# Kernel optimization log

Hardware: AMD Instinct MI355X
Metric: run time of the kernel (lower is better)

Reference implementation:

```python
import jax, jax.numpy as jnp
import numpy as np

NVAR, B, C, H, W = 3, 4, 256, 64, 64
C1 = C // 2          # dat channels (nc)
C2 = C - C1
HEADS = 4
HC = C1 // HEADS     # head channels
STRIDE = 4
KS = 4
HK, WK = H // STRIDE, W // STRIDE
NS = HK * WK         # n_sample
RPE_H, RPE_W = 2 * H - 1, 2 * W - 1
NPAIR = 3


def _grid_sample(img, grid):
    # img [B,C,Hi,Wi]; grid [B,Hg,Wg,2] = (x,y) in [-1,1]; bilinear, align_corners=True, zero-pad
    Bn, Cn, Hi, Wi = img.shape
    x = (grid[..., 0] + 1.0) * 0.5 * (Wi - 1)
    y = (grid[..., 1] + 1.0) * 0.5 * (Hi - 1)
    x0 = jnp.floor(x)
    y0 = jnp.floor(y)
    wx = x - x0
    wy = y - y0
    x0i = x0.astype(jnp.int32)
    y0i = y0.astype(jnp.int32)
    imt = img.transpose(0, 2, 3, 1)  # [B,Hi,Wi,C]
    bidx = jnp.arange(Bn)[:, None, None]

    def corner(yi, xi, wgt):
        ok = ((xi >= 0) & (xi < Wi) & (yi >= 0) & (yi < Hi)).astype(img.dtype)
        val = imt[bidx, jnp.clip(yi, 0, Hi - 1), jnp.clip(xi, 0, Wi - 1)]  # [B,Hg,Wg,C]
        return val * (wgt * ok)[..., None]

    out = (corner(y0i, x0i, (1 - wx) * (1 - wy))
           + corner(y0i, x0i + 1, wx * (1 - wy))
           + corner(y0i + 1, x0i, (1 - wx) * wy)
           + corner(y0i + 1, x0i + 1, wx * wy))
    return out.transpose(0, 3, 1, 2)  # [B,C,Hg,Wg]


def _ref_points(hk, wk):
    # normalized sampling-grid reference points, (y,x) order
    ry = (jnp.linspace(0.5, hk - 0.5, hk) / (hk - 1.0)) * 2.0 - 1.0
    rx = (jnp.linspace(0.5, wk - 0.5, wk) / (wk - 1.0)) * 2.0 - 1.0
    return jnp.stack(jnp.meshgrid(ry, rx, indexing='ij'), axis=-1)  # [hk,wk,2]


def _q_grid(h, w):
    gy = (jnp.arange(h, dtype=jnp.float32) / (h - 1.0)) * 2.0 - 1.0
    gx = (jnp.arange(w, dtype=jnp.float32) / (w - 1.0)) * 2.0 - 1.0
    return jnp.stack(jnp.meshgrid(gy, gx, indexing='ij'), axis=-1).reshape(h * w, 2)


def _conv1x1(x, w, b=None):
    y = jnp.einsum('oc,bchw->bohw', w, x)
    return y if b is None else y + b[None, :, None, None]


def _dat_block(q_in, kv_in, pWq, pbq, pWk, pbk, pWv, pbv, pWo, pbo,
               pdw_w, pdw_b, pln_g, pln_b, ppw_w, prpe):
    Bn = q_in.shape[0]
    q = _conv1x1(q_in, pWq, pbq)  # [B,C1,H,W]
    # offset net: depthwise 4x4 stride-4 conv -> channel LN -> GELU -> 1x1 conv to 2
    off = jax.lax.conv_general_dilated(
        q, pdw_w, (STRIDE, STRIDE), 'VALID',
        dimension_numbers=('NCHW', 'OIHW', 'NCHW'),
        feature_group_count=C1) + pdw_b[None, :, None, None]  # [B,C1,HK,WK]
    mu = off.mean(axis=1, keepdims=True)
    var = ((off - mu) ** 2).mean(axis=1, keepdims=True)
    off = (off - mu) * jax.lax.rsqrt(var + 1e-5) * pln_g[None, :, None, None] + pln_b[None, :, None, None]
    off = jax.nn.gelu(off, approximate=False)
    offset = _conv1x1(off, ppw_w).transpose(0, 2, 3, 1)  # [B,HK,WK,2] (dy,dx)
    # offset_range_factor = -1 -> no tanh scaling, clamp pos into [-1,1]
    pos = jnp.clip(offset + _ref_points(HK, WK)[None], -1.0, 1.0)  # [B,HK,WK,2]
    xs = _grid_sample(kv_in, pos[..., ::-1])  # sample kv at deformed points -> [B,C1,HK,WK]
    k = _conv1x1(xs, pWk, pbk).reshape(Bn, HEADS, HC, NS)
    v = _conv1x1(xs, pWv, pbv).reshape(Bn, HEADS, HC, NS)
    qh = q.reshape(Bn, HEADS, HC, H * W)
    attn = jnp.einsum('bhcm,bhcn->bhmn', qh, k) * (HC ** -0.5)  # [B,h,HW,NS]
    # relative position bias sampled from rpe table
    disp = (_q_grid(H, W)[None, :, None, :] - pos.reshape(Bn, 1, NS, 2)) * 0.5  # [B,HW,NS,2]
    rpe_b = jnp.broadcast_to(prpe[None], (Bn, HEADS, RPE_H, RPE_W))
    bias = _grid_sample(rpe_b, disp[..., ::-1])  # [B,h,HW,NS]
    attn = jax.nn.softmax(attn + bias, axis=-1)
    out = jnp.einsum('bhmn,bhcn->bhcm', attn, v).reshape(Bn, C1, H, W)
    return _conv1x1(out, pWo, pbo)


def _forward(xs, params):
    results = []
    num = 0
    for i in range(NVAR):
        res = xs[i]
        for j in range(i):
            attn_out = _dat_block(xs[i][:, :C1], xs[j][:, :C1],
                                  *(p[num] for p in params))
            # torch: res -= -cat(zeros[:,:C2], attn)  => add attn on channels C2:
            res = res.at[:, C2:].add(attn_out)
            num += 1
        results.append(res)
    return jnp.stack(results)  # [NVAR,B,C,H,W]


def setup_inputs() -> dict:
    key = jax.random.key(0)
    ks = jax.random.split(key, 4)
    d = {}
    for n, k in zip(['x0', 'x1', 'x2'], jax.random.split(ks[0], 3)):
        d[n] = jax.random.normal(k, (B, C, H, W), jnp.float32)

    def w(k, shape, s=0.02):
        return jax.random.normal(k, shape, jnp.float32) * s

    kk = jax.random.split(ks[1], 8)
    d['Wq'] = w(kk[0], (NPAIR, C1, C1))
    d['bq'] = jnp.zeros((NPAIR, C1), jnp.float32)
    d['Wk'] = w(kk[1], (NPAIR, C1, C1))
    d['bk'] = jnp.zeros((NPAIR, C1), jnp.float32)
    d['Wv'] = w(kk[2], (NPAIR, C1, C1))
    d['bv'] = jnp.zeros((NPAIR, C1), jnp.float32)
    d['Wo'] = w(kk[3], (NPAIR, C1, C1))
    d['bo'] = jnp.zeros((NPAIR, C1), jnp.float32)
    d['dw_w'] = w(kk[4], (NPAIR, C1, 1, KS, KS), 0.1)
    d['dw_b'] = jnp.zeros((NPAIR, C1), jnp.float32)
    d['ln_g'] = jnp.ones((NPAIR, C1), jnp.float32)
    d['ln_b'] = jnp.zeros((NPAIR, C1), jnp.float32)
    d['pw_w'] = w(kk[5], (NPAIR, 2, C1), 0.1)
    d['rpe'] = w(kk[6], (NPAIR, HEADS, RPE_H, RPE_W), 0.01)
    return d


def reference(x0, x1, x2, Wq, bq, Wk, bk, Wv, bv, Wo, bo,
              dw_w, dw_b, ln_g, ln_b, pw_w, rpe):
    params = (Wq, bq, Wk, bk, Wv, bv, Wo, bo, dw_w, dw_b, ln_g, ln_b, pw_w, rpe)
    out = _forward([x0, x1, x2], params)
    flow = jnp.zeros((NVAR, x0.shape[0]), out.dtype)
    return out, flow
```

## Files before the change

kernel.cpp:

```cpp
#include <hip/hip_runtime.h>
#include <math.h>

#define NVAR 3
#define BB 4
#define CC 256
#define C1 128
#define HEADS 4
#define HH 64
#define WW 64
#define HW 4096
#define RPE_W 127
#define NP 3
#define SCALE 0.17677669529663687f

typedef short bf16x8 __attribute__((ext_vector_type(8)));
typedef float f32x4 __attribute__((ext_vector_type(4)));
typedef __bf16 bf16x2 __attribute__((ext_vector_type(2)));

__device__ __forceinline__ unsigned short f2bf(float f) {
    unsigned int u = __float_as_uint(f);
    u += 0x7fffu + ((u >> 16) & 1u);
    return (unsigned short)(u >> 16);
}
__device__ __forceinline__ float bflo(unsigned u) { return __uint_as_float(u << 16); }
__device__ __forceinline__ float bfhi(unsigned u) { return __uint_as_float(u & 0xffff0000u); }

__device__ __forceinline__ float dot2bf(unsigned a, unsigned b, float c) {
#if __has_builtin(__builtin_amdgcn_fdot2_f32_bf16)
    return __builtin_amdgcn_fdot2_f32_bf16(__builtin_bit_cast(bf16x2, a),
                                           __builtin_bit_cast(bf16x2, b), c, false);
#else
    return c + bflo(a) * bflo(b) + bfhi(a) * bfhi(b);
#endif
}

__global__ __launch_bounds__(256) void prep_copy(const float* __restrict__ rpe,
                                                 const float* __restrict__ Wq,
                                                 const float* __restrict__ Wo,
                                                 const float* __restrict__ Wk,
                                                 const float* __restrict__ Wv,
                                                 const float* __restrict__ x0,
                                                 unsigned short* __restrict__ tabbf,
                                                 unsigned short* __restrict__ wqh,
                                                 unsigned short* __restrict__ wql,
                                                 unsigned short* __restrict__ woh,
                                                 unsigned short* __restrict__ wkh,
                                                 unsigned short* __restrict__ wvh,
                                                 float* __restrict__ out) {
    int blk = blockIdx.x;
    if (blk >= 24) {
        const long long n4 = (long long)BB * CC * HW / 4;
        long long i = (long long)(blk - 24) * 256 + threadIdx.x;
        const long long stride = 1024LL * 256;
        for (; i < n4 + 12; i += stride) {
            if (i < n4) ((float4*)out)[i] = ((const float4*)x0)[i];
            else out[3LL * BB * CC * HW + (i - n4)] = 0.f;
        }
        return;
    }
    if (blk < 12) {
        const float* src = rpe + (long long)blk * RPE_W * RPE_W;
        unsigned short* dst = tabbf + (long long)blk * 16384;
        for (int idx = threadIdx.x; idx < 16384; idx += 256) {
            int y = idx >> 7, x = idx & 127;
            float v = (y < RPE_W && x < RPE_W) ? src[y * RPE_W + x] : 0.f;
            dst[idx] = f2bf(v);
        }
    } else if (blk < 15) {
        int p = blk - 12;
        for (int i = threadIdx.x; i < 16384; i += 256) {
            float w = Wq[p * 16384 + i];
            unsigned short h = f2bf(w);
            wqh[p * 16384 + i] = h;
            wql[p * 16384 + i] = f2bf(w - bflo((unsigned)h));
        }
    } else if (blk < 18) {
        int p = blk - 15;
        for (int i = threadIdx.x; i < 16384; i += 256)
            woh[p * 16384 + i] = f2bf(Wo[p * 16384 + i]);
    } else if (blk < 21) {
        int p = blk - 18;
        for (int i = threadIdx.x; i < 16384; i += 256)
            wkh[p * 16384 + i] = f2bf(Wk[p * 16384 + i]);
    } else {
        int p = blk - 21;
        for (int i = threadIdx.x; i < 16384; i += 256)
            wvh[p * 16384 + i] = f2bf(Wv[p * 16384 + i]);
    }
}

__global__ __launch_bounds__(256) void conv_q(const float* __restrict__ x1,
                                              const float* __restrict__ x2,
                                              const unsigned short* __restrict__ wqh,
                                              const unsigned short* __restrict__ wql,
                                              const float* __restrict__ bq,
                                              float* __restrict__ qbuf,
                                              unsigned short* __restrict__ qbf,
                                              float* __restrict__ out) {
    __shared__ unsigned short qlds[4][16][136];
    int wid = threadIdx.x >> 6, lane = threadIdx.x & 63;
    int g = lane >> 4, lm = lane & 15;
    int gw = blockIdx.x * 4 + wid;
    int mt = gw & 255;
    int pb = gw >> 8;
    int p = pb >> 2, b = pb & 3;
    const float* X = ((p == 0) ? x1 : x2) + (long long)b * CC * HW;
    int m = mt * 16 + lm;
    float* outc = (p < 2)
        ? out + (((long long)((p + 1) * 4 + b)) * CC) * HW + m
        : nullptr;

    bf16x8 bhi[4], blo[4];
#pragma unroll
    for (int ksl = 0; ksl < 4; ksl++) {
        float v[8];
#pragma unroll
        for (int j = 0; j < 8; j++) {
            int k = ksl * 32 + 8 * g + j;
            v[j] = X[(long long)k * HW + m];
            if (outc) outc[(long long)k * HW] = v[j];
        }
        union { unsigned u[4]; bf16x8 v; } H, L;
#pragma unroll
        for (int t = 0; t < 4; t++) {
            unsigned short h0 = f2bf(v[2 * t]), h1 = f2bf(v[2 * t + 1]);
            unsigned short l0 = f2bf(v[2 * t] - bflo((unsigned)h0));
            unsigned short l1 = f2bf(v[2 * t + 1] - bflo((unsigned)h1));
            H.u[t] = (unsigned)h0 | ((unsigned)h1 << 16);
            L.u[t] = (unsigned)l0 | ((unsigned)l1 << 16);
        }
        bhi[ksl] = H.v;
        blo[ksl] = L.v;
    }

    const unsigned short* WH = wqh + p * 16384;
    const unsigned short* WL = wql + p * 16384;
    unsigned short* ql = &qlds[wid][lm][0];
    f32x4 zero = {0.f, 0.f, 0.f, 0.f};
#pragma unroll
    for (int ct2 = 0; ct2 < 4; ct2++) {
        int ct0 = 2 * ct2, ct1 = ct0 + 1;
        f32x4 a0 = zero, a1 = zero;
#pragma unroll
        for (int ksl = 0; ksl < 4; ksl++) {
            bf16x8 Ah0 = *(const bf16x8*)(WH + (ct0 * 16 + lm) * 128 + ksl * 32 + 8 * g);
            bf16x8 Al0 = *(const bf16x8*)(WL + (ct0 * 16 + lm) * 128 + ksl * 32 + 8 * g);
            bf16x8 Ah1 = *(const bf16x8*)(WH + (ct1 * 16 + lm) * 128 + ksl * 32 + 8 * g);
            bf16x8 Al1 = *(const bf16x8*)(WL + (ct1 * 16 + lm) * 128 + ksl * 32 + 8 * g);
            a0 = __builtin_amdgcn_mfma_f32_16x16x32_bf16(Ah0, bhi[ksl], a0, 0, 0, 0);
            a1 = __builtin_amdgcn_mfma_f32_16x16x32_bf16(Ah1, bhi[ksl], a1, 0, 0, 0);
            a0 = __builtin_amdgcn_mfma_f32_16x16x32_bf16(Ah0, blo[ksl], a0, 0, 0, 0);
            a1 = __builtin_amdgcn_mfma_f32_16x16x32_bf16(Ah1, blo[ksl], a1, 0, 0, 0);
            a0 = __builtin_amdgcn_mfma_f32_16x16x32_bf16(Al0, bhi[ksl], a0, 0, 0, 0);
            a1 = __builtin_amdgcn_mfma_f32_16x16x32_bf16(Al1, bhi[ksl], a1, 0, 0, 0);
        }
        float q0[4], q1[4];
#pragma unroll
        for (int r = 0; r < 4; r++) {
            int c0 = ct0 * 16 + 4 * g + r, c1 = ct1 * 16 + 4 * g + r;
            q0[r] = a0[r] + bq[p * 128 + c0];
            q1[r] = a1[r] + bq[p * 128 + c1];
            qbuf[((long long)pb * 128 + c0) * HW + m] = q0[r];
            qbuf[((long long)pb * 128 + c1) * HW + m] = q1[r];
        }
        *(unsigned*)(ql + ct0 * 16 + 4 * g) =
            (unsigned)f2bf(q0[0] * SCALE) | ((unsigned)f2bf(q0[1] * SCALE) << 16);
        *(unsigned*)(ql + ct0 * 16 + 4 * g + 2) =
            (unsigned)f2bf(q0[2] * SCALE) | ((unsigned)f2bf(q0[3] * SCALE) << 16);
        *(unsigned*)(ql + ct1 * 16 + 4 * g) =
            (unsigned)f2bf(q1[0] * SCALE) | ((unsigned)f2bf(q1[1] * SCALE) << 16);
        *(unsigned*)(ql + ct1 * 16 + 4 * g + 2) =
            (unsigned)f2bf(q1[2] * SCALE) | ((unsigned)f2bf(q1[3] * SCALE) << 16);
    }

    unsigned short* Yb = qbf + ((long long)pb * HW + mt * 16) * 128;
    int q = lane >> 4, cg = lane & 15;
#pragma unroll
    for (int i = 0; i < 4; i++) {
        int row = i * 4 + q;
        uint4 vv = *(const uint4*)&qlds[wid][row][cg * 8];
        *(uint4*)(Yb + row * 128 + cg * 8) = vv;
    }
}

__global__ __launch_bounds__(256) void mid_kernel(const float* __restrict__ qbuf,
                                                  const float* __restrict__ dw_w,
                                                  const float* __restrict__ dw_b,
                                                  const float* __restrict__ ln_g,
                                                  const float* __restrict__ ln_b,
                                                  const float* __restrict__ pw_w,
                                                  const float* __restrict__ x0,
                                                  const float* __restrict__ x1,
                                                  float* __restrict__ posb,
                                                  uint4* __restrict__ prmb,
                                                  unsigned short* __restrict__ xT) {
    __shared__ float sm[32 * 4 * 65 + 16 * 128];
    int blk = blockIdx.x;
    int tid = threadIdx.x;
    if (blk < 192) {
        float (*ld)[4][65] = (float(*)[4][65])sm;
        float (*dwout)[128] = (float(*)[128])(sm + 32 * 4 * 65);
        int pb = blk >> 4, hk = blk & 15;
        int p = pb >> 2;
        for (int cq = 0; cq < 4; cq++) {
            int c32 = cq * 32;
            __syncthreads();
#pragma unroll
            for (int it = 0; it < 8; it++) {
                int i2 = tid + it * 256;
                int c = i2 >> 6, rem = i2 & 63;
                int y = rem >> 4, xq = rem & 15;
                float4 v = *(const float4*)(qbuf + ((long long)pb * 128 + c32 + c) * HW
                                            + (4 * hk + y) * 64 + xq * 4);
                ld[c][y][xq * 4 + 0] = v.x;
                ld[c][y][xq * 4 + 1] = v.y;
                ld[c][y][xq * 4 + 2] = v.z;
                ld[c][y][xq * 4 + 3] = v.w;
            }
            __syncthreads();
            int wk = tid >> 4;
#pragma unroll
            for (int oi = 0; oi < 2; oi++) {
                int c = (tid & 15) + oi * 16;
                const float* dwp = dw_w + (p * 128 + c32 + c) * 16;
                float acc = dw_b[p * 128 + c32 + c];
#pragma unroll
                for (int ky = 0; ky < 4; ky++)
#pragma unroll
                    for (int kx = 0; kx < 4; kx++)
                        acc += ld[c][ky][wk * 4 + kx] * dwp[ky * 4 + kx];
                dwout[wk][c32 + c] = acc;
            }
        }
        __syncthreads();
        int wid = tid >> 6, lane = tid & 63;
        for (int i = 0; i < 4; i++) {
            int wk = wid * 4 + i;
            int s = hk * 16 + wk;
            float a0 = dwout[wk][lane], a1 = dwout[wk][lane + 64];
            float s1 = a0 + a1;
#pragma unroll
            for (int o = 1; o < 64; o <<= 1) s1 += __shfl_xor(s1, o);
            float mu = s1 * (1.f / 128.f);
            float d0 = a0 - mu, d1 = a1 - mu;
            float v2 = d0 * d0 + d1 * d1;
#pragma unroll
            for (int o = 1; o < 64; o <<= 1) v2 += __shfl_xor(v2, o);
            float rs = rsqrtf(v2 * (1.f / 128.f) + 1e-5f);
            int c0 = lane, c1 = lane + 64;
            float y0 = d0 * rs * ln_g[p * 128 + c0] + ln_b[p * 128 + c0];
            float y1 = d1 * rs * ln_g[p * 128 + c1] + ln_b[p * 128 + c1];
            float g0 = 0.5f * y0 * (1.f + erff(y0 * 0.70710678118654752f));
            float g1 = 0.5f * y1 * (1.f + erff(y1 * 0.70710678118654752f));
            float o0 = pw_w[(p * 2 + 0) * 128 + c0] * g0
                     + pw_w[(p * 2 + 0) * 128 + c1] * g1;
            float o1 = pw_w[(p * 2 + 1) * 128 + c0] * g0
                     + pw_w[(p * 2 + 1) * 128 + c1] * g1;
#pragma unroll
            for (int o = 1; o < 64; o <<= 1) o0 += __shfl_xor(o0, o);
#pragma unroll
            for (int o = 1; o < 64; o <<= 1) o1 += __shfl_xor(o1, o);
            if (lane == 0) {
                int wk2 = s & 15;
                float refy = (hk + 0.5f) * (2.f / 15.f) - 1.f;
                float refx = (wk2 + 0.5f) * (2.f / 15.f) - 1.f;
                float py = fminf(fmaxf(o0 + refy, -1.f), 1.f);
                float px = fminf(fmaxf(o1 + refx, -1.f), 1.f);
                int pbn = pb * 256 + s;
                posb[pbn * 2 + 0] = py;
                posb[pbn * 2 + 1] = px;
                float cy = 31.5f * (1.f - py), cx = 31.5f * (1.f - px);
                float yf = floorf(cy), xf = floorf(cx);
                float wy = cy - yf, wx = cx - xf;
                int Y0 = (int)yf, X0 = (int)xf;
                uint4 v;
                v.x = (unsigned)f2bf((1.f - wy) * (1.f - wx))
                    | ((unsigned)f2bf((1.f - wy) * wx) << 16);
                v.y = (unsigned)f2bf(wy * (1.f - wx))
                    | ((unsigned)f2bf(wy * wx) << 16);
                v.z = (unsigned)((Y0 * 128 + X0) * 2);
                v.w = 0;
                prmb[pbn] = v;
            }
        }
    } else {
        float (*ld2)[65] = (float(*)[65])sm;
        int rem = blk - 192;
        int v = rem >> 10;
        int rem1 = rem & 1023;
        int b = rem1 >> 8;
        int rem2 = rem1 & 255;
        int ct = rem2 >> 6;
        int mt = rem2 & 63;
        const float* src = ((v == 0) ? x0 : x1) + (long long)b * CC * HW
                           + (long long)(ct * 32) * HW + mt * 64;
#pragma unroll
        for (int it = 0; it < 2; it++) {
            int c = tid >> 3, x4 = (tid & 7) + it * 8;
            float4 w = *(const float4*)(src + (long long)c * HW + x4 * 4);
            ld2[c][x4 * 4 + 0] = w.x;
            ld2[c][x4 * 4 + 1] = w.y;
            ld2[c][x4 * 4 + 2] = w.z;
            ld2[c][x4 * 4 + 3] = w.w;
        }
        __syncthreads();
        int m = tid >> 2, cg = tid & 3;
        union { unsigned u[4]; } pk;
#pragma unroll
        for (int t = 0; t < 4; t++) {
            unsigned short h0 = f2bf(ld2[cg * 8 + 2 * t][m]);
            unsigned short h1 = f2bf(ld2[cg * 8 + 2 * t + 1][m]);
            pk.u[t] = (unsigned)h0 | ((unsigned)h1 << 16);
        }
        *(uint4*)(xT + (((long long)(v * 4 + b)) * HW + mt * 64 + m) * 128
                  + ct * 32 + cg * 8) = *(uint4*)pk.u;
    }
}

__global__ __launch_bounds__(256) void sample_kv(const unsigned short* __restrict__ xT,
                                                 const float* __restrict__ posb,
                                                 const unsigned short* __restrict__ wkh,
                                                 const unsigned short* __restrict__ wvh,
                                                 const float* __restrict__ bk,
                                                 const float* __restrict__ bv,
                                                 unsigned short* __restrict__ kbf,
                                                 unsigned short* __restrict__ vbf) {
    __shared__ unsigned short xls[32 * 128];
    int blk = blockIdx.x;
    int pb = blk >> 3;
    int nt = blk & 7;
    int p = pb >> 2, b = pb & 3;
    int n0 = nt * 32;
    int tid = threadIdx.x;

    {
        int nl = tid >> 3, co = tid & 7;
        int n = n0 + nl;
        float py = posb[(pb * 256 + n) * 2 + 0];
        float px = posb[(pb * 256 + n) * 2 + 1];
        float yi = (py + 1.f) * 31.5f, xi = (px + 1.f) * 31.5f;
        yi = fminf(fmaxf(yi, 0.f), 63.f);
        xi = fminf(fmaxf(xi, 0.f), 63.f);
        int y0 = min((int)yi, 62);
        int x0i = min((int)xi, 62);
        float wy = yi - (float)y0, wx = xi - (float)x0i;
        float w00 = (1.f - wy) * (1.f - wx), w01 = (1.f - wy) * wx;
        float w10 = wy * (1.f - wx), w11 = wy * wx;
        int vsel = (p == 2) ? 1 : 0;
        const unsigned short* base = xT + ((long long)(vsel * 4 + b)) * HW * 128;
        int m00 = y0 * 64 + x0i;
        char* dst = (char*)xls;
#pragma unroll
        for (int cb = 0; cb < 2; cb++) {
            int c0 = co * 16 + cb * 8;
            bf16x8 a = *(const bf16x8*)(base + (long long)m00 * 128 + c0);
            bf16x8 bb = *(const bf16x8*)(base + (long long)(m00 + 1) * 128 + c0);
            bf16x8 cc = *(const bf16x8*)(base + (long long)(m00 + 64) * 128 + c0);
            bf16x8 dd = *(const bf16x8*)(base + (long long)(m00 + 65) * 128 + c0);
            union { unsigned u[4]; bf16x8 v; } R;
#pragma unroll
            for (int t = 0; t < 4; t++) {
                float r0 = w00 * bflo((unsigned)(unsigned short)a[2 * t])
                         + w01 * bflo((unsigned)(unsigned short)bb[2 * t])
                         + w10 * bflo((unsigned)(unsigned short)cc[2 * t])
                         + w11 * bflo((unsigned)(unsigned short)dd[2 * t]);
                float r1 = w00 * bflo((unsigned)(unsigned short)a[2 * t + 1])
                         + w01 * bflo((unsigned)(unsigned short)bb[2 * t + 1])
                         + w10 * bflo((unsigned)(unsigned short)cc[2 * t + 1])
                         + w11 * bflo((unsigned)(unsigned short)dd[2 * t + 1]);
                R.u[t] = (unsigned)f2bf(r0) | ((unsigned)f2bf(r1) << 16);
            }
            *(bf16x8*)(dst + ((nl * 256 + c0 * 2) ^ ((nl & 7) << 4))) = R.v;
        }
    }
    __syncthreads();

    int wid = tid >> 6, lane = tid & 63;
    int g = lane >> 4, lm = lane & 15;
    int ntile = wid & 1, isv = wid >> 1;
    int nl = ntile * 16 + lm;
    const char* srcl = (const char*)xls;
    bf16x8 xf[4];
#pragma unroll
    for (int ks = 0; ks < 4; ks++)
        xf[ks] = *(const bf16x8*)(srcl + ((nl * 256 + (ks * 32 + 8 * g) * 2)
                                          ^ ((nl & 7) << 4)));
    f32x4 zero = {0.f, 0.f, 0.f, 0.f};
    if (!isv) {
        const unsigned short* WK = wkh + p * 16384;
#pragma unroll
        for (int ct = 0; ct < 8; ct++) {
            f32x4 acc = zero;
#pragma unroll
            for (int ks = 0; ks < 4; ks++) {
                bf16x8 wf = *(const bf16x8*)(WK + (ct * 16 + lm) * 128 + ks * 32 + 8 * g);
                acc = __builtin_amdgcn_mfma_f32_16x16x32_bf16(xf[ks], wf, acc, 0, 0, 0);
            }
            float bias = bk[p * 128 + ct * 16 + lm];
#pragma unroll
            for (int r = 0; r < 4; r++) {
                int n = n0 + ntile * 16 + 4 * g + r;
                kbf[((long long)pb * 256 + n) * 128 + ct * 16 + lm] = f2bf(acc[r] + bias);
            }
        }
    } else {
        const unsigned short* WV = wvh + p * 16384;
#pragma unroll
        for (int ct = 0; ct < 8; ct++) {
            f32x4 acc = zero;
#pragma unroll
            for (int ks = 0; ks < 4; ks++) {
                bf16x8 wf = *(const bf16x8*)(WV + (ct * 16 + lm) * 128 + ks * 32 + 8 * g);
                acc = __builtin_amdgcn_mfma_f32_16x16x32_bf16(wf, xf[ks], acc, 0, 0, 0);
            }
#pragma unroll
            for (int r = 0; r < 4; r++) {
                int c = ct * 16 + 4 * g + r;
                vbf[((long long)pb * 128 + c) * 256 + n0 + ntile * 16 + lm]
                    = f2bf(acc[r] + bv[p * 128 + c]);
            }
        }
    }
}

__global__ __launch_bounds__(256, 4) void attn_mfma(
        const unsigned short* __restrict__ qbf,
        const unsigned short* __restrict__ kbf,
        const unsigned short* __restrict__ vbf,
        const unsigned short* __restrict__ tabbf,
        const uint4* __restrict__ prmb,
        float* __restrict__ obuf) {
    __shared__ unsigned short tab[16384 + 8];
    __shared__ uint4 prm[256];
    int tid = threadIdx.x;
    int wid = tid >> 6, lane = tid & 63;
    int g = lane >> 4, lm = lane & 15;
    int bid = blockIdx.x;
    int my = bid & 63;
    int h = (bid >> 6) & 3;
    int b = (bid >> 8) & 3;
    int p = bid >> 10;
    int pb = p * 4 + b;

    {
        const uint4* ts = (const uint4*)(tabbf + (long long)(p * 4 + h) * 16384);
        uint4* td = (uint4*)tab;
#pragma unroll
        for (int i = 0; i < 8; i++) td[tid + i * 256] = ts[tid + i * 256];
        prm[tid] = prmb[pb * 256 + tid];
    }
    __syncthreads();

    int mx = (wid << 4) + lm;

    bf16x8 qf = *(const bf16x8*)(qbf + ((long long)pb * HW + my * 64 + mx) * 128
                                 + h * 32 + 8 * g);
    const unsigned short* kbase = kbf + ((long long)pb * 256 + lm) * 128
                                  + h * 32 + 8 * g;
    f32x4 zero = {0.f, 0.f, 0.f, 0.f};
    f32x4 acc[16];
    __builtin_amdgcn_s_setprio(1);
#pragma unroll
    for (int ni = 0; ni < 16; ni++) {
        bf16x8 kf = *(const bf16x8*)(kbase + ni * 16 * 128);
        acc[ni] = __builtin_amdgcn_mfma_f32_16x16x32_bf16(kf, qf, zero, 0, 0, 0);
    }
    __builtin_amdgcn_s_setprio(0);

    int laneoff = (my * 128 + mx) * 2;
    const char* tb = (const char*)tab;
#pragma unroll
    for (int ni = 0; ni < 16; ni++) {
#pragma unroll
        for (int r = 0; r < 4; r++) {
            int n = ni * 16 + 4 * g + r;
            uint4 pw = prm[n];
            int va = (int)pw.z + laneoff;
            int va4 = va & ~3;
            int sh = va & 3;
            unsigned r0 = *(const unsigned*)(tb + va4);
            unsigned r1 = *(const unsigned*)(tb + va4 + 4);
            unsigned r2 = *(const unsigned*)(tb + va4 + 256);
            unsigned r3 = *(const unsigned*)(tb + va4 + 260);
            unsigned p0 = __builtin_amdgcn_alignbyte(r1, r0, sh);
            unsigned p1 = __builtin_amdgcn_alignbyte(r3, r2, sh);
            float t = acc[ni][r];
            t = dot2bf(p0, pw.x, t);
            t = dot2bf(p1, pw.y, t);
            acc[ni][r] = t;
        }
    }

    float mxv = -1e30f;
#pragma unroll
    for (int ni = 0; ni < 16; ni++)
        mxv = fmaxf(mxv, fmaxf(fmaxf(acc[ni][0], acc[ni][1]),
                               fmaxf(acc[ni][2], acc[ni][3])));
    mxv = fmaxf(mxv, __shfl_xor(mxv, 16));
    mxv = fmaxf(mxv, __shfl_xor(mxv, 32));
    float sum = 0.f;
    unsigned dwA[16], dwB[16];
#pragma unroll
    for (int ni = 0; ni < 16; ni++) {
        float e0 = __expf(acc[ni][0] - mxv);
        float e1 = __expf(acc[ni][1] - mxv);
        float e2 = __expf(acc[ni][2] - mxv);
        float e3 = __expf(acc[ni][3] - mxv);
        sum += (e0 + e1) + (e2 + e3);
        asm("v_cvt_pk_bf16_f32 %0, %1, %2" : "=v"(dwA[ni]) : "v"(e0), "v"(e1));
        asm("v_cvt_pk_bf16_f32 %0, %1, %2" : "=v"(dwB[ni]) : "v"(e2), "v"(e3));
    }
    sum += __shfl_xor(sum, 16);
    sum += __shfl_xor(sum, 32);

    int src0 = ((g & 1) << 5) + lm;
    int src1 = src0 + 16;
    bool sel = (g >> 1) != 0;
    const unsigned short* vb0 = vbf + ((long long)pb * 128 + h * 32 + lm) * 256
                                + 8 * g;
    f32x4 o0 = zero, o1 = zero;
#pragma unroll
    for (int st = 0; st < 8; st++) {
        unsigned d0a = __shfl(dwA[2 * st], src0), d0b = __shfl(dwA[2 * st + 1], src0);
        unsigned d1a = __shfl(dwB[2 * st], src0), d1b = __shfl(dwB[2 * st + 1], src0);
        unsigned d2a = __shfl(dwA[2 * st], src1), d2b = __shfl(dwA[2 * st + 1], src1);
        unsigned d3a = __shfl(dwB[2 * st], src1), d3b = __shfl(dwB[2 * st + 1], src1);
        union { unsigned u[4]; bf16x8 v; } pf;
        pf.u[0] = sel ? d0b : d0a;
        pf.u[1] = sel ? d1b : d1a;
        pf.u[2] = sel ? d2b : d2a;
        pf.u[3] = sel ? d3b : d3a;
        bf16x8 v0 = *(const bf16x8*)(vb0 + st * 32);
        bf16x8 v1 = *(const bf16x8*)(vb0 + 4096 + st * 32);
        __builtin_amdgcn_s_setprio(1);
        o0 = __builtin_amdgcn_mfma_f32_16x16x32_bf16(v0, pf.v, o0, 0, 0, 0);
        o1 = __builtin_amdgcn_mfma_f32_16x16x32_bf16(v1, pf.v, o1, 0, 0, 0);
        __builtin_amdgcn_s_setprio(0);
    }

    float inv = 1.f / sum;
    float* ob = obuf + ((long long)pb * 128 + h * 32) * HW + my * 64 + mx;
#pragma unroll
    for (int r = 0; r < 4; r++) {
        ob[(g * 4 + r) * HW] = o0[r] * inv;
        ob[(16 + g * 4 + r) * HW] = o1[r] * inv;
    }
}

__global__ __launch_bounds__(256) void conv_wo(const float* __restrict__ x1,
                                               const float* __restrict__ x2,
                                               const float* __restrict__ obuf,
                                               const unsigned short* __restrict__ woh,
                                               const float* __restrict__ bo,
                                               float* __restrict__ out) {
    int wid = threadIdx.x >> 6, lane = threadIdx.x & 63;
    int g = lane >> 4, lm = lane & 15;
    int gw = blockIdx.x * 4 + wid;
    int mt = gw & 255;
    int b = (gw >> 8) & 3;
    int vs = gw >> 10;
    int m = mt * 16 + lm;
    int np = vs + 1;

    f32x4 acc[8];
#pragma unroll
    for (int ct = 0; ct < 8; ct++) acc[ct] = (f32x4){0.f, 0.f, 0.f, 0.f};

    for (int pi = 0; pi < np; pi++) {
        int p = vs ? (1 + pi) : 0;
        const float* O = obuf + (long long)(p * 4 + b) * 128 * HW;
        bf16x8 bh[4];
#pragma unroll
        for (int ksl = 0; ksl < 4; ksl++) {
            float v[8];
#pragma unroll
            for (int j = 0; j < 8; j++)
                v[j] = O[(long long)(ksl * 32 + 8 * g + j) * HW + m];
            union { unsigned u[4]; bf16x8 v; } H;
#pragma unroll
            for (int t = 0; t < 4; t++)
                H.u[t] = (unsigned)f2bf(v[2 * t]) | ((unsigned)f2bf(v[2 * t + 1]) << 16);
            bh[ksl] = H.v;
        }
        const unsigned short* WH = woh + p * 16384;
#pragma unroll
        for (int ct = 0; ct < 8; ct++)
#pragma unroll
            for (int ksl = 0; ksl < 4; ksl++) {
                bf16x8 A = *(const bf16x8*)(WH + (ct * 16 + lm) * 128 + ksl * 32 + 8 * g);
                acc[ct] = __builtin_amdgcn_mfma_f32_16x16x32_bf16(A, bh[ksl], acc[ct], 0, 0, 0);
            }
    }

    int qi = vs + 1;
    const float* xq = (vs ? x2 : x1) + (long long)b * CC * HW;
#pragma unroll
    for (int ct = 0; ct < 8; ct++)
#pragma unroll
        for (int r = 0; r < 4; r++) {
            int c = ct * 16 + 4 * g + r;
            float bias = vs ? (bo[128 + c] + bo[256 + c]) : bo[c];
            float base = xq[(long long)(128 + c) * HW + m];
            out[(((long long)(qi * 4 + b)) * CC + 128 + c) * HW + m]
                = base + acc[ct][r] + bias;
        }
}

extern "C" void kernel_launch(void* const* d_in, const int* in_sizes, int n_in,
                              void* d_out, int out_size, void* d_ws, size_t ws_size,
                              hipStream_t stream) {
    const float* x0 = (const float*)d_in[0];
    const float* x1 = (const float*)d_in[1];
    const float* x2 = (const float*)d_in[2];
    const float* Wq = (const float*)d_in[3];
    const float* bq = (const float*)d_in[4];
    const float* Wk = (const float*)d_in[5];
    const float* bk = (const float*)d_in[6];
    const float* Wv = (const float*)d_in[7];
    const float* bv = (const float*)d_in[8];
    const float* Wo = (const float*)d_in[9];
    const float* bo = (const float*)d_in[10];
    const float* dw_w = (const float*)d_in[11];
    const float* dw_b = (const float*)d_in[12];
    const float* ln_g = (const float*)d_in[13];
    const float* ln_b = (const float*)d_in[14];
    const float* pw_w = (const float*)d_in[15];
    const float* rpe = (const float*)d_in[16];
    float* out = (float*)d_out;

    float* ws = (float*)d_ws;
    float* qbuf = ws;
    float* obuf = qbuf;
    float* posb = ws + 6291456;
    unsigned short* xT = (unsigned short*)(posb + 6144);
    unsigned short* qbf = xT + 4194304;
    unsigned short* kbf = qbf + 12582912;
    unsigned short* vbf = kbf + 393216;
    unsigned short* tabbf = vbf + 393216;
    uint4* prmb = (uint4*)(tabbf + 196608);
    unsigned short* wqh = (unsigned short*)(prmb + 3072);
    unsigned short* wql = wqh + 49152;
    unsigned short* woh = wql + 49152;
    unsigned short* wkh = woh + 49152;
    unsigned short* wvh = wkh + 49152;

    prep_copy<<<1048, 256, 0, stream>>>(rpe, Wq, Wo, Wk, Wv, x0, tabbf,
                                        wqh, wql, woh, wkh, wvh, out);
    conv_q<<<768, 256, 0, stream>>>(x1, x2, wqh, wql, bq, qbuf, qbf, out);
    mid_kernel<<<2240, 256, 0, stream>>>(qbuf, dw_w, dw_b, ln_g, ln_b, pw_w,
                                         x0, x1, posb, prmb, xT);
    sample_kv<<<96, 256, 0, stream>>>(xT, posb, wkh, wvh, bk, bv, kbf, vbf);
    attn_mfma<<<3072, 256, 0, stream>>>(qbf, kbf, vbf, tabbf, prmb, obuf);
    conv_wo<<<512, 256, 0, stream>>>(x1, x2, obuf, woh, bo, out);
}
```

Measured before the change: 180.6 us.

## Store attention output as bf16 pixel-major via LDS transpose for conv_wo

The attention kernel now converts its output to bf16 and stages it through shared memory, then writes it in a pixel-major [pb, pixel, 128-channel] layout with 16-byte stores. Previously it wrote fp32 channel-major values with strided scalar stores. conv_wo now reads that buffer directly as bf16x8 vectors instead of gathering eight strided fp32 values per fragment and converting them. This halves intermediate traffic and makes both the writes and the reads contiguous, at the cost of an extra __syncthreads and LDS staging in attn_mfma. The bf16 rounding point is unchanged because conv_wo already rounded to bf16.

```diff
diff --git a/kernel.cpp b/kernel.cpp
--- a/kernel.cpp
+++ b/kernel.cpp
@@ -429,7 +429,7 @@
         const unsigned short* __restrict__ vbf,
         const unsigned short* __restrict__ tabbf,
         const uint4* __restrict__ prmb,
-        float* __restrict__ obuf) {
+        unsigned short* __restrict__ obf) {
     __shared__ unsigned short tab[16384 + 8];
     __shared__ uint4 prm[256];
     int tid = threadIdx.x;
@@ -539,17 +539,27 @@
     }
 
     float inv = 1.f / sum;
-    float* ob = obuf + ((long long)pb * 128 + h * 32) * HW + my * 64 + mx;
-#pragma unroll
-    for (int r = 0; r < 4; r++) {
-        ob[(g * 4 + r) * HW] = o0[r] * inv;
-        ob[(16 + g * 4 + r) * HW] = o1[r] * inv;
-    }
+    __syncthreads();
+    {
+        unsigned short* rw = tab + wid * 640 + lm * 40;
+        *(unsigned*)(rw + g * 4) =
+            (unsigned)f2bf(o0[0] * inv) | ((unsigned)f2bf(o0[1] * inv) << 16);
+        *(unsigned*)(rw + g * 4 + 2) =
+            (unsigned)f2bf(o0[2] * inv) | ((unsigned)f2bf(o0[3] * inv) << 16);
+        *(unsigned*)(rw + 16 + g * 4) =
+            (unsigned)f2bf(o1[0] * inv) | ((unsigned)f2bf(o1[1] * inv) << 16);
+        *(unsigned*)(rw + 16 + g * 4 + 2) =
+            (unsigned)f2bf(o1[2] * inv) | ((unsigned)f2bf(o1[3] * inv) << 16);
+    }
+    int row = lane >> 2, cb = lane & 3;
+    uint4 vv = *(const uint4*)(tab + wid * 640 + row * 40 + cb * 8);
+    *(uint4*)(obf + ((long long)pb * HW + my * 64 + wid * 16 + row) * 128
+              + h * 32 + cb * 8) = vv;
 }
 
 __global__ __launch_bounds__(256) void conv_wo(const float* __restrict__ x1,
                                                const float* __restrict__ x2,
-                                               const float* __restrict__ obuf,
+                                               const unsigned short* __restrict__ obf,
                                                const unsigned short* __restrict__ woh,
                                                const float* __restrict__ bo,
                                                float* __restrict__ out) {
@@ -568,28 +578,17 @@
 
     for (int pi = 0; pi < np; pi++) {
         int p = vs ? (1 + pi) : 0;
-        const float* O = obuf + (long long)(p * 4 + b) * 128 * HW;
-        bf16x8 bh[4];
+        const unsigned short* Om = obf + ((long long)(p * 4 + b) * HW + m) * 128;
+        const unsigned short* WH = woh + p * 16384;
 #pragma unroll
         for (int ksl = 0; ksl < 4; ksl++) {
-            float v[8];
-#pragma unroll
-            for (int j = 0; j < 8; j++)
-                v[j] = O[(long long)(ksl * 32 + 8 * g + j) * HW + m];
-            union { unsigned u[4]; bf16x8 v; } H;
-#pragma unroll
-            for (int t = 0; t < 4; t++)
-                H.u[t] = (unsigned)f2bf(v[2 * t]) | ((unsigned)f2bf(v[2 * t + 1]) << 16);
-            bh[ksl] = H.v;
-        }
-        const unsigned short* WH = woh + p * 16384;
-#pragma unroll
-        for (int ct = 0; ct < 8; ct++)
-#pragma unroll
-            for (int ksl = 0; ksl < 4; ksl++) {
+            bf16x8 bh = *(const bf16x8*)(Om + ksl * 32 + 8 * g);
+#pragma unroll
+            for (int ct = 0; ct < 8; ct++) {
                 bf16x8 A = *(const bf16x8*)(WH + (ct * 16 + lm) * 128 + ksl * 32 + 8 * g);
-                acc[ct] = __builtin_amdgcn_mfma_f32_16x16x32_bf16(A, bh[ksl], acc[ct], 0, 0, 0);
-            }
+                acc[ct] = __builtin_amdgcn_mfma_f32_16x16x32_bf16(A, bh, acc[ct], 0, 0, 0);
+            }
+        }
     }
 
     int qi = vs + 1;
@@ -630,7 +629,7 @@
 
     float* ws = (float*)d_ws;
     float* qbuf = ws;
-    float* obuf = qbuf;
+    unsigned short* obf = (unsigned short*)ws;
     float* posb = ws + 6291456;
     unsigned short* xT = (unsigned short*)(posb + 6144);
     unsigned short* qbf = xT + 4194304;
@@ -650,6 +649,6 @@
     mid_kernel<<<2240, 256, 0, stream>>>(qbuf, dw_w, dw_b, ln_g, ln_b, pw_w,
                                          x0, x1, posb, prmb, xT);
     sample_kv<<<96, 256, 0, stream>>>(xT, posb, wkh, wvh, bk, bv, kbf, vbf);
-    attn_mfma<<<3072, 256, 0, stream>>>(qbf, kbf, vbf, tabbf, prmb, obuf);
-    conv_wo<<<512, 256, 0, stream>>>(x1, x2, obuf, woh, bo, out);
-}
+    attn_mfma<<<3072, 256, 0, stream>>>(qbf, kbf, vbf, tabbf, prmb, obf);
+    conv_wo<<<512, 256, 0, stream>>>(x1, x2, obf, woh, bo, out);
+}
```

Result: no change. 178.9 us (-1.0%).
